# Kernel tuning notes

Hardware: AMD Instinct MI355X
Metric: run time of the kernel (lower is better)

## Reference

```python
import jax, jax.numpy as jnp
import numpy as np

N_WORD = 50000
N_DOC = 10000
E_WW = 800000
E_WD = 320000


def _sage(h_src, h_dst, src, dst, n_dst, W_self, W_neigh, b):
    # DGL SAGEConv('mean'): fc_self(h_dst) + fc_neigh(mean_{u in N(v)} h_u) + bias
    ones = jnp.ones((src.shape[0],), dtype=h_src.dtype)
    deg = jax.ops.segment_sum(ones, dst, num_segments=n_dst)            # [n_dst]
    agg = jax.ops.segment_sum(h_src[src], dst, num_segments=n_dst)      # [n_dst, d]
    mean = agg / jnp.maximum(deg, 1.0)[:, None]                          # zero for isolated
    return h_dst @ W_self + mean @ W_neigh + b


def _layer(xw, xd, edges, Ws, Wn, b):
    (ww_s, ww_d, wwr_s, wwr_d, wd_s, wd_d, wdr_s, wdr_d) = edges
    # relations targeting 'word': word2word, word2wordr, word2documentr
    h_ww = _sage(xw, xw, ww_s, ww_d, N_WORD, Ws[0], Wn[0], b[0])
    h_wwr = _sage(xw, xw, wwr_s, wwr_d, N_WORD, Ws[1], Wn[1], b[1])
    h_wdr = _sage(xd, xw, wdr_s, wdr_d, N_WORD, Ws[3], Wn[3], b[3])
    # relation targeting 'document': word2document
    h_wd = _sage(xw, xd, wd_s, wd_d, N_DOC, Ws[2], Wn[2], b[2])
    # HeteroGraphConv aggregate='stack' then torch.sum(dim=1) == sum over relations; then relu
    return jax.nn.relu(h_ww + h_wwr + h_wdr), jax.nn.relu(h_wd)


def setup_inputs() -> dict:
    key = jax.random.key(0)
    ks = jax.random.split(key, 20)
    d_in, d_h = 256, 128
    inp = {
        "x_word": jax.random.normal(ks[0], (N_WORD, d_in), jnp.float32),
        "x_doc": jax.random.normal(ks[1], (N_DOC, d_in), jnp.float32),
        "ww_src": jax.random.randint(ks[2], (E_WW,), 0, N_WORD, jnp.int32),
        "ww_dst": jax.random.randint(ks[3], (E_WW,), 0, N_WORD, jnp.int32),
        "wwr_src": jax.random.randint(ks[4], (E_WW,), 0, N_WORD, jnp.int32),
        "wwr_dst": jax.random.randint(ks[5], (E_WW,), 0, N_WORD, jnp.int32),
        "wd_src": jax.random.randint(ks[6], (E_WD,), 0, N_WORD, jnp.int32),
        "wd_dst": jax.random.randint(ks[7], (E_WD,), 0, N_DOC, jnp.int32),
        "wdr_src": jax.random.randint(ks[8], (E_WD,), 0, N_DOC, jnp.int32),
        "wdr_dst": jax.random.randint(ks[9], (E_WD,), 0, N_WORD, jnp.int32),
        "Wself1": jax.random.normal(ks[10], (4, d_in, d_h), jnp.float32) * (1.0 / np.sqrt(d_in)),
        "Wneigh1": jax.random.normal(ks[11], (4, d_in, d_h), jnp.float32) * (1.0 / np.sqrt(d_in)),
        "b1": jnp.zeros((4, d_h), jnp.float32),
        "Wself2": jax.random.normal(ks[12], (4, d_h, d_h), jnp.float32) * (1.0 / np.sqrt(d_h)),
        "Wneigh2": jax.random.normal(ks[13], (4, d_h, d_h), jnp.float32) * (1.0 / np.sqrt(d_h)),
        "b2": jnp.zeros((4, d_h), jnp.float32),
        "lin_w": jax.random.normal(ks[14], (1, d_h), jnp.float32) * (1.0 / np.sqrt(d_h)),
        "lin_b": jnp.ones((1,), jnp.float32),
    }
    return inp


def reference(x_word, x_doc, ww_src, ww_dst, wwr_src, wwr_dst, wd_src, wd_dst,
              wdr_src, wdr_dst, Wself1, Wneigh1, b1, Wself2, Wneigh2, b2, lin_w, lin_b):
    edges = (ww_src, ww_dst, wwr_src, wwr_dst, wd_src, wd_dst, wdr_src, wdr_dst)
    xw, xd = _layer(x_word, x_doc, edges, Wself1, Wneigh1, b1)
    xw, xd = _layer(xw, xd, edges, Wself2, Wneigh2, b2)
    out_w = jax.nn.sigmoid(xw @ lin_w.T + lin_b)  # [N_WORD, 1]
    out_d = jax.nn.sigmoid(xd @ lin_w.T + lin_b)  # [N_DOC, 1]
    return out_w, out_d
```

## Files before the change

kernel.cpp:

```cpp
#include <hip/hip_runtime.h>
#include <math.h>

#define N_WORD 50000
#define N_DOC  10000
#define E_WW   800000
#define E_WD   320000
#define D_IN   256
#define D_H    128

#define NPB    256
#define NBK_W  196
#define NBK_D  40
#define BKT    (3 * NBK_W + NBK_D)
#define EPB    8192
#define NBLK_WW 98
#define NBLK_WD 40
#define NBLK_TOT (2 * NBLK_WW + 2 * NBLK_WD)
#define PACK_BLKS 145

#define CAP_WW  4736
#define CAP_WDR 2176
#define CAP_WD  8960

#define WSTRIP ((N_WORD + 63) / 64)
#define DSTRIP ((N_DOC + 63) / 64)
#define NSTRIP (WSTRIP + DSTRIP)

typedef __attribute__((ext_vector_type(8))) short short8;
typedef __attribute__((ext_vector_type(4))) float f32x4;
typedef __attribute__((ext_vector_type(2))) float f32x2;

__device__ inline unsigned short f2bf(float f) {
  unsigned u = __float_as_uint(f);
  u = (u + 0x7fffu + ((u >> 16) & 1u)) >> 16;
  return (unsigned short)u;
}

__device__ inline float bflo(unsigned u) { return __uint_as_float(u << 16); }
__device__ inline float bfhi(unsigned u) { return __uint_as_float(u & 0xffff0000u); }

struct G6 { const short* B[6]; unsigned short* C[6]; };

#define BCH 16384
#define W2SZ 16384

template <int ABF, int K>
__device__ void gemm_body(const void* __restrict__ Aw, const void* __restrict__ Ad,
                          const G6& g, int blk, short* __restrict__ Bs) {
  constexpr int KT = K >> 5;
  constexpr int NCH = KT / 4;
  int tid = threadIdx.x;
  int wid = tid >> 6, lane = tid & 63;
  const void* A; int M, row0, h0, h1;
  if (blk < WSTRIP) { A = Aw; M = N_WORD; row0 = blk << 6; h0 = 0; h1 = 4; }
  else { A = Ad; M = N_DOC; row0 = (blk - WSTRIP) << 6; h0 = 4; h1 = 6; }
  int r = lane & 15, quad = lane >> 4;
  int m0 = row0 + wid * 16;
  int mA = m0 + r; if (mA >= M) mA = M - 1;
  short8 afr[KT];
  if (ABF) {
    const short* ap = (const short*)A + (size_t)mA * K + quad * 8;
#pragma unroll
    for (int kt = 0; kt < KT; ++kt) afr[kt] = *(const short8*)(ap + kt * 32);
  } else {
    const float* ap = (const float*)A + (size_t)mA * K + quad * 8;
#pragma unroll
    for (int kt = 0; kt < KT; ++kt) {
      float4 a0 = *(const float4*)(ap + kt * 32);
      float4 a1 = *(const float4*)(ap + kt * 32 + 4);
      short8 v;
      v[0] = (short)f2bf(a0.x); v[1] = (short)f2bf(a0.y);
      v[2] = (short)f2bf(a0.z); v[3] = (short)f2bf(a0.w);
      v[4] = (short)f2bf(a1.x); v[5] = (short)f2bf(a1.y);
      v[6] = (short)f2bf(a1.z); v[7] = (short)f2bf(a1.w);
      afr[kt] = v;
    }
  }
  for (int h = h0; h < h1; ++h) {
    const short* Bp = g.B[h];
    f32x4 acc[8];
#pragma unroll
    for (int nt = 0; nt < 8; ++nt) acc[nt] = (f32x4){0.f, 0.f, 0.f, 0.f};
    for (int c = 0; c < NCH; ++c) {
      const short* src = Bp + (size_t)c * BCH;
#pragma unroll
      for (int i = 0; i < 8; ++i) {
        int o = (i * 256 + tid) * 8;
        *(short8*)(Bs + o) = *(const short8*)(src + o);
      }
      __syncthreads();
#pragma unroll
      for (int ktl = 0; ktl < 4; ++ktl) {
        const short* bbase = Bs + ktl * 4096 + lane * 8;
#pragma unroll
        for (int nt = 0; nt < 8; ++nt) {
          short8 bf = *(const short8*)(bbase + nt * 512);
          acc[nt] = __builtin_amdgcn_mfma_f32_16x16x32_bf16(afr[c * 4 + ktl], bf, acc[nt], 0, 0, 0);
        }
      }
      __syncthreads();
    }
    unsigned short* C = g.C[h];
#pragma unroll
    for (int nt = 0; nt < 8; ++nt)
#pragma unroll
      for (int rr = 0; rr < 4; ++rr) {
        int row = m0 + quad * 4 + rr;
        if (row < M) C[(size_t)row * 128 + nt * 16 + r] = f2bf(acc[nt][rr]);
      }
  }
}

template <int NS>
__device__ void gemm2_fused(const unsigned* A0, const unsigned* A1,
                            const unsigned* A2, const unsigned* A3,
                            const short* B0, const short* B1,
                            const short* B2, const short* B3,
                            int M, int row0, const float* __restrict__ bias, int ob,
                            const float* __restrict__ lw, const float* __restrict__ lb,
                            float* __restrict__ out, short* __restrict__ Bs) {
  const unsigned* As[4] = {A0, A1, A2, A3};
  const short* Bm[4] = {B0, B1, B2, B3};
  int tid = threadIdx.x;
  int wid = tid >> 6, lane = tid & 63;
  int r = lane & 15, quad = lane >> 4;
  int m0 = row0 + wid * 16;
  int mA = m0 + r; if (mA >= M) mA = M - 1;
  short8 afr[NS][4];
#pragma unroll
  for (int s = 0; s < NS; ++s) {
    const short* ap = (const short*)As[s] + (size_t)mA * 128 + quad * 8;
#pragma unroll
    for (int kt = 0; kt < 4; ++kt) afr[s][kt] = *(const short8*)(ap + kt * 32);
  }
  f32x4 acc[8];
#pragma unroll
  for (int nt = 0; nt < 8; ++nt) acc[nt] = (f32x4){0.f, 0.f, 0.f, 0.f};
#pragma unroll
  for (int s = 0; s < NS; ++s) {
    const short* src = Bm[s];
#pragma unroll
    for (int i = 0; i < 8; ++i) {
      int o = (i * 256 + tid) * 8;
      *(short8*)(Bs + o) = *(const short8*)(src + o);
    }
    __syncthreads();
#pragma unroll
    for (int ktl = 0; ktl < 4; ++ktl) {
      const short* bbase = Bs + ktl * 4096 + lane * 8;
#pragma unroll
      for (int nt = 0; nt < 8; ++nt) {
        short8 bf = *(const short8*)(bbase + nt * 512);
        acc[nt] = __builtin_amdgcn_mfma_f32_16x16x32_bf16(afr[s][ktl], bf, acc[nt], 0, 0, 0);
      }
    }
    __syncthreads();
  }
  float bsv[8], lwv[8];
#pragma unroll
  for (int nt = 0; nt < 8; ++nt) { bsv[nt] = bias[nt * 16 + r]; lwv[nt] = lw[nt * 16 + r]; }
  float lbv = lb[0];
#pragma unroll
  for (int rr = 0; rr < 4; ++rr) {
    float p = 0.f;
#pragma unroll
    for (int nt = 0; nt < 8; ++nt) {
      float v = acc[nt][rr] + bsv[nt];
      v = fmaxf(v, 0.f);
      p += v * lwv[nt];
    }
    p += __shfl_xor(p, 1, 64);
    p += __shfl_xor(p, 2, 64);
    p += __shfl_xor(p, 4, 64);
    p += __shfl_xor(p, 8, 64);
    int row = m0 + quad * 4 + rr;
    if (r == 0 && row < M) out[ob + row] = 1.0f / (1.0f + expf(-(p + lbv)));
  }
}

__global__ __launch_bounds__(256, 2) void gemm2f_kernel(
    const unsigned* __restrict__ x1w, const unsigned* __restrict__ x1d,
    const unsigned* __restrict__ mww, const unsigned* __restrict__ mwwr,
    const unsigned* __restrict__ mwdr, const unsigned* __restrict__ mwd,
    const short* __restrict__ Bp2, const float* __restrict__ bsW,
    const float* __restrict__ bsD, const float* __restrict__ lw,
    const float* __restrict__ lb, float* __restrict__ out) {
  __shared__ short Bs[W2SZ];
  int blk = blockIdx.x;
  if (blk < WSTRIP)
    gemm2_fused<4>(x1w, mww, mwwr, mwdr,
                   Bp2, Bp2 + W2SZ, Bp2 + 2 * W2SZ, Bp2 + 4 * W2SZ,
                   N_WORD, blk << 6, bsW, 0, lw, lb, out, Bs);
  else
    gemm2_fused<2>(x1d, mwd, nullptr, nullptr,
                   Bp2 + 5 * W2SZ, Bp2 + 3 * W2SZ, nullptr, nullptr,
                   N_DOC, (blk - WSTRIP) << 6, bsD, N_WORD, lw, lb, out, Bs);
}

__global__ __launch_bounds__(256) void prep_kernel(
    const float* __restrict__ Ws1, const float* __restrict__ Wn1,
    const float* __restrict__ Ws2, const float* __restrict__ Wn2,
    short* __restrict__ Bp1, short* __restrict__ Bp2,
    const float* __restrict__ b1, const float* __restrict__ b2,
    float* __restrict__ bs1, float* __restrict__ bs2, int* __restrict__ bcnt,
    unsigned* __restrict__ zA, unsigned* __restrict__ zB,
    unsigned* __restrict__ zC, unsigned* __restrict__ zD,
    unsigned* __restrict__ zE, unsigned* __restrict__ zF) {
  int b = blockIdx.x;
  if (b == PACK_BLKS) {
    for (int i = threadIdx.x; i < BKT; i += 256) bcnt[i] = 0;
    if (threadIdx.x < 64) {
      zA[(size_t)N_WORD * 64 + threadIdx.x] = 0;
      zB[(size_t)N_WORD * 64 + threadIdx.x] = 0;
      zC[(size_t)N_WORD * 64 + threadIdx.x] = 0;
      zD[(size_t)N_DOC * 64 + threadIdx.x] = 0;
      zE[(size_t)N_WORD * 64 + threadIdx.x] = 0;
      zF[(size_t)N_DOC * 64 + threadIdx.x] = 0;
    }
    return;
  }
  int tid = b * 256 + threadIdx.x;
  const int L1T = 6 * 4096;
  const int L2T = 6 * 2048;
  if (tid >= L1T + L2T) {
    int t = tid - (L1T + L2T);
    if (t < 128) bs1[t] = b1[t] + b1[128 + t] + b1[384 + t];
    else if (t < 256) { int u = t - 128; bs2[u] = b2[u] + b2[128 + u] + b2[384 + u]; }
    return;
  }
  const float *src0, *src1 = nullptr, *src2 = nullptr;
  short* dstp;
  int kt, nt, lane;
  if (tid < L1T) {
    int mat = tid / 4096, rem = tid % 4096;
    kt = rem / 512; nt = (rem / 64) % 8; lane = rem % 64;
    const int W1 = 256 * 128;
    if (mat == 0) { src0 = Ws1; src1 = Ws1 + W1; src2 = Ws1 + 3 * W1; }
    else if (mat <= 4) src0 = Wn1 + (size_t)(mat - 1) * W1;
    else src0 = Ws1 + 2 * W1;
    dstp = Bp1 + (size_t)mat * W1 + ((size_t)(kt * 8 + nt) * 64 + lane) * 8;
  } else {
    int t2 = tid - L1T;
    int mat = t2 / 2048, rem = t2 % 2048;
    kt = rem / 512; nt = (rem / 64) % 8; lane = rem % 64;
    if (mat == 0) { src0 = Ws2; src1 = Ws2 + W2SZ; src2 = Ws2 + 3 * W2SZ; }
    else if (mat <= 4) src0 = Wn2 + (size_t)(mat - 1) * W2SZ;
    else src0 = Ws2 + 2 * W2SZ;
    dstp = Bp2 + (size_t)mat * W2SZ + ((size_t)(kt * 8 + nt) * 64 + lane) * 8;
  }
  int n = nt * 16 + (lane & 15);
  int kb = kt * 32 + (lane >> 4) * 8;
  short8 v;
#pragma unroll
  for (int j = 0; j < 8; ++j) {
    float f = src0[(size_t)(kb + j) * 128 + n];
    if (src1) f += src1[(size_t)(kb + j) * 128 + n] + src2[(size_t)(kb + j) * 128 + n];
    v[j] = (short)f2bf(f);
  }
  *(short8*)dstp = v;
}

__device__ inline void rel_map(int b, const int* wwd, const int* wwrd, const int* wdrd,
                               const int* wdd, const int*& dst, int& E, int& gbase, int& lb) {
  if (b < NBLK_WW) { dst = wwd; E = E_WW; gbase = 0; lb = b; }
  else if (b < 2 * NBLK_WW) { dst = wwrd; E = E_WW; gbase = NBK_W; lb = b - NBLK_WW; }
  else if (b < 2 * NBLK_WW + NBLK_WD) { dst = wdrd; E = E_WD; gbase = 2 * NBK_W; lb = b - 2 * NBLK_WW; }
  else { dst = wdd; E = E_WD; gbase = 3 * NBK_W; lb = b - 2 * NBLK_WW - NBLK_WD; }
}

struct BinLDS {
  unsigned buf[EPB];
  int hist[NBK_W];
  int lofs[NBK_W];
  int gofs[NBK_W];
  int lcur[NBK_W];
  int sm[256];
};

union FusedLDS {
  BinLDS bin;
  short bs[BCH];
};

__global__ __launch_bounds__(256, 4) void bin_gemm1(
    const int* wws, const int* wwd, const int* wwrs, const int* wwrd,
    const int* wdrs, const int* wdrd, const int* wds, const int* wdd,
    int* bcnt, unsigned* st_ww, unsigned* st_wwr, unsigned* st_wdr, unsigned* st_wd,
    const float* __restrict__ Aw, const float* __restrict__ Ad, G6 g) {
  __shared__ FusedLDS U;
  int b = blockIdx.x;
  if (b >= NBLK_TOT) {
    gemm_body<0, 256>(Aw, Ad, g, b - NBLK_TOT, U.bs);
    return;
  }
  BinLDS& L = U.bin;
  const int* dst; int E, gbase, lb;
  rel_map(b, wwd, wwrd, wdrd, wdd, dst, E, gbase, lb);
  const int* src; unsigned* st; int cap;
  if (b < NBLK_WW) { src = wws; st = st_ww; cap = CAP_WW; }
  else if (b < 2 * NBLK_WW) { src = wwrs; st = st_wwr; cap = CAP_WW; }
  else if (b < 2 * NBLK_WW + NBLK_WD) { src = wdrs; st = st_wdr; cap = CAP_WDR; }
  else { src = wds; st = st_wd; cap = CAP_WD; }
  int tid = threadIdx.x;
  int e0 = lb * EPB;
  int ecnt = E - e0; if (ecnt > EPB) ecnt = EPB;
  if (tid < NBK_W) L.hist[tid] = 0;
  __syncthreads();
  int dcache[EPB / 256];
#pragma unroll
  for (int k = 0; k < EPB / 256; ++k) {
    int i = e0 + k * 256 + tid;
    int d = (i < E) ? dst[i] : -1;
    dcache[k] = d;
    if (d >= 0) atomicAdd(&L.hist[d >> 8], 1);
  }
  __syncthreads();
  {
    int v = (tid < NBK_W) ? L.hist[tid] : 0;
    L.sm[tid] = v;
    __syncthreads();
    for (int o = 1; o < 256; o <<= 1) {
      int add = (tid >= o) ? L.sm[tid - o] : 0;
      __syncthreads();
      L.sm[tid] += add;
      __syncthreads();
    }
    if (tid < NBK_W) {
      int ex = L.sm[tid] - v;
      L.lofs[tid] = ex;
      L.lcur[tid] = ex;
      int base = v ? atomicAdd(&bcnt[gbase + tid], v) : 0;
      L.gofs[tid] = (int)((size_t)tid * cap) + base - ex;
    }
  }
  __syncthreads();
#pragma unroll
  for (int k = 0; k < EPB / 256; ++k) {
    int d = dcache[k];
    if (d >= 0) {
      int i = e0 + k * 256 + tid;
      int bk = d >> 8;
      int p = atomicAdd(&L.lcur[bk], 1);
      L.buf[p] = ((unsigned)bk << 24) | ((unsigned)(d & 255) << 16) |
                 (unsigned)(src[i] & 0xFFFF);
    }
  }
  __syncthreads();
#pragma unroll
  for (int k = 0; k < EPB / 256; ++k) {
    int p = k * 256 + tid;
    if (p < ecnt) {
      unsigned e = L.buf[p];
      st[L.gofs[e >> 24] + p] = e & 0x00FFFFFFu;
    }
  }
}

struct CSRB {
  const unsigned *st_ww, *st_wwr, *st_wdr, *st_wd;
  unsigned short *c_ww, *c_wwr, *c_wdr, *c_wd;
  int *rp_ww, *rp_wwr, *rp_wdr, *rp_wd;
  const int* bcnt;
};

__global__ __launch_bounds__(256) void place_kernel(CSRB q) {
  __shared__ int cnt[256], off[256], sm[256];
  int g = blockIdx.x;
  const unsigned* st; unsigned short* csr; int* rp; int relFirst, relLast, n, cap, Etot;
  if (g < NBK_W)            { st = q.st_ww;  csr = q.c_ww;  rp = q.rp_ww;  relFirst = 0;         relLast = NBK_W - 1;     n = N_WORD; cap = CAP_WW;  Etot = E_WW; }
  else if (g < 2 * NBK_W)   { st = q.st_wwr; csr = q.c_wwr; rp = q.rp_wwr; relFirst = NBK_W;     relLast = 2 * NBK_W - 1; n = N_WORD; cap = CAP_WW;  Etot = E_WW; }
  else if (g < 3 * NBK_W)   { st = q.st_wdr; csr = q.c_wdr; rp = q.rp_wdr; relFirst = 2 * NBK_W; relLast = 3 * NBK_W - 1; n = N_WORD; cap = CAP_WDR; Etot = E_WD; }
  else                      { st = q.st_wd;  csr = q.c_wd;  rp = q.rp_wd;  relFirst = 3 * NBK_W; relLast = BKT - 1;       n = N_DOC;  cap = CAP_WD;  Etot = E_WD; }
  int cb = g - relFirst;
  int tid = threadIdx.x;
  int v = (tid < cb) ? q.bcnt[relFirst + tid] : 0;
  sm[tid] = v;
  __syncthreads();
  for (int o = 128; o > 0; o >>= 1) {
    if (tid < o) sm[tid] += sm[tid + o];
    __syncthreads();
  }
  int bstart = sm[0];
  if (g == relLast && tid == 0) rp[n] = Etot;
  __syncthreads();
  int node_base = cb << 8;
  int node_cnt = n - node_base; if (node_cnt > NPB) node_cnt = NPB;
  int ecnt = q.bcnt[g];
  const unsigned* w = st + (size_t)cb * cap;
  cnt[tid] = 0;
  __syncthreads();
  for (int j = tid; j < ecnt; j += 256) atomicAdd(&cnt[w[j] >> 16], 1);
  __syncthreads();
  int c = cnt[tid];
  sm[tid] = c;
  __syncthreads();
  for (int o = 1; o < 256; o <<= 1) {
    int add = (tid >= o) ? sm[tid - o] : 0;
    __syncthreads();
    sm[tid] += add;
    __syncthreads();
  }
  int ex = sm[tid] - c;
  off[tid] = ex;
  if (tid < node_cnt) rp[node_base + tid] = bstart + ex;
  __syncthreads();
  for (int j = tid; j < ecnt; j += 256) {
    unsigned e = w[j];
    int p = atomicAdd(&off[e >> 16], 1);
    csr[bstart + p] = (unsigned short)(e & 0xFFFFu);
  }
}

__device__ inline void accum_rel4(const uint4* __restrict__ Y,
                                  const unsigned short* __restrict__ csr,
                                  int beg, int end, int lane, int r, int g,
                                  int zrow, f32x2* __restrict__ f) {
  int deg = end - beg;
  if (deg <= 0) return;
  f32x2 a0 = {0.f, 0.f}, a1 = a0, a2 = a0, a3 = a0;
  for (int base = beg; base < end; base += 64) {
    int cnt = end - base; if (cnt > 64) cnt = 64;
    int ld = base + lane;
    int idx = (ld < end) ? (int)csr[ld] : zrow;
    for (int j = 0; j < cnt; j += 16) {
      uint4 u[4];
#pragma unroll
      for (int t = 0; t < 4; ++t) {
        int sv = __shfl(idx, j + (t << 2) + g, 64);
        u[t] = Y[(unsigned)((sv << 4) + r)];
      }
#pragma unroll
      for (int t = 0; t < 4; ++t) {
        a0 += (f32x2){bflo(u[t].x), bfhi(u[t].x)};
        a1 += (f32x2){bflo(u[t].y), bfhi(u[t].y)};
        a2 += (f32x2){bflo(u[t].z), bfhi(u[t].z)};
        a3 += (f32x2){bflo(u[t].w), bfhi(u[t].w)};
      }
    }
  }
  float inv = 1.0f / (float)deg;
  f[0] += a0 * inv; f[1] += a1 * inv; f[2] += a2 * inv; f[3] += a3 * inv;
}

__global__ __launch_bounds__(256) void gather_all(
    const unsigned* __restrict__ y_ww, const unsigned* __restrict__ y_wwr,
    const unsigned* __restrict__ y_wdr, const unsigned* __restrict__ y_wd,
    const unsigned short* __restrict__ c_ww, const unsigned short* __restrict__ c_wwr,
    const unsigned short* __restrict__ c_wdr, const unsigned short* __restrict__ c_wd,
    const int* __restrict__ r_ww, const int* __restrict__ r_wwr,
    const int* __restrict__ r_wdr, const int* __restrict__ r_wd,
    const unsigned* __restrict__ tW, const unsigned* __restrict__ tD,
    const float* __restrict__ bW, const float* __restrict__ bD,
    unsigned* __restrict__ oW16, unsigned* __restrict__ oD16) {
  int gn = (blockIdx.x << 2) + (threadIdx.x >> 6);
  if (gn >= N_WORD + N_DOC) return;
  int lane = threadIdx.x & 63;
  int r = lane & 15, g = lane >> 4;
  f32x2 f[4];
#pragma unroll
  for (int i = 0; i < 4; ++i) f[i] = (f32x2){0.f, 0.f};
  bool isw = (gn < N_WORD);
  int node = isw ? gn : gn - N_WORD;
  if (isw) {
    accum_rel4((const uint4*)y_ww, c_ww, r_ww[node], r_ww[node + 1], lane, r, g, N_WORD, f);
    accum_rel4((const uint4*)y_wwr, c_wwr, r_wwr[node], r_wwr[node + 1], lane, r, g, N_WORD, f);
    accum_rel4((const uint4*)y_wdr, c_wdr, r_wdr[node], r_wdr[node + 1], lane, r, g, N_DOC, f);
  } else {
    accum_rel4((const uint4*)y_wd, c_wd, r_wd[node], r_wd[node + 1], lane, r, g, N_WORD, f);
  }
#pragma unroll
  for (int i = 0; i < 4; ++i) {
    f[i].x += __shfl_xor(f[i].x, 16, 64);
    f[i].y += __shfl_xor(f[i].y, 16, 64);
    f[i].x += __shfl_xor(f[i].x, 32, 64);
    f[i].y += __shfl_xor(f[i].y, 32, 64);
  }
  const unsigned* tS = isw ? tW : tD;
  uint4 tu = ((const uint4*)tS)[(unsigned)((node << 4) + r)];
  const float* bs = isw ? bW : bD;
  float4 bv0 = ((const float4*)bs)[2 * r];
  float4 bv1 = ((const float4*)bs)[2 * r + 1];
  f[0].x = fmaxf(f[0].x + bflo(tu.x) + bv0.x, 0.f);
  f[0].y = fmaxf(f[0].y + bfhi(tu.x) + bv0.y, 0.f);
  f[1].x = fmaxf(f[1].x + bflo(tu.y) + bv0.z, 0.f);
  f[1].y = fmaxf(f[1].y + bfhi(tu.y) + bv0.w, 0.f);
  f[2].x = fmaxf(f[2].x + bflo(tu.z) + bv1.x, 0.f);
  f[2].y = fmaxf(f[2].y + bfhi(tu.z) + bv1.y, 0.f);
  f[3].x = fmaxf(f[3].x + bflo(tu.w) + bv1.z, 0.f);
  f[3].y = fmaxf(f[3].y + bfhi(tu.w) + bv1.w, 0.f);
  if (g == 0) {
    uint4 pk;
    pk.x = (unsigned)f2bf(f[0].x) | ((unsigned)f2bf(f[0].y) << 16);
    pk.y = (unsigned)f2bf(f[1].x) | ((unsigned)f2bf(f[1].y) << 16);
    pk.z = (unsigned)f2bf(f[2].x) | ((unsigned)f2bf(f[2].y) << 16);
    pk.w = (unsigned)f2bf(f[3].x) | ((unsigned)f2bf(f[3].y) << 16);
    unsigned* o = isw ? oW16 : oD16;
    ((uint4*)o)[(unsigned)((node << 4) + r)] = pk;
  }
}

__device__ inline void mean_write(int node, int lane, int r, int g,
                                  f32x2* __restrict__ A, unsigned* __restrict__ mT) {
#pragma unroll
  for (int i = 0; i < 4; ++i) {
    A[i].x += __shfl_xor(A[i].x, 16, 64);
    A[i].y += __shfl_xor(A[i].y, 16, 64);
    A[i].x += __shfl_xor(A[i].x, 32, 64);
    A[i].y += __shfl_xor(A[i].y, 32, 64);
  }
  if (g == 0) {
    uint4 pk;
    pk.x = (unsigned)f2bf(A[0].x) | ((unsigned)f2bf(A[0].y) << 16);
    pk.y = (unsigned)f2bf(A[1].x) | ((unsigned)f2bf(A[1].y) << 16);
    pk.z = (unsigned)f2bf(A[2].x) | ((unsigned)f2bf(A[2].y) << 16);
    pk.w = (unsigned)f2bf(A[3].x) | ((unsigned)f2bf(A[3].y) << 16);
    ((uint4*)mT)[(unsigned)((node << 4) + r)] = pk;
  }
}

__global__ __launch_bounds__(256) void gather_mean(
    const unsigned* __restrict__ yW, const unsigned* __restrict__ yD,
    const unsigned short* __restrict__ c_ww, const unsigned short* __restrict__ c_wwr,
    const unsigned short* __restrict__ c_wdr, const unsigned short* __restrict__ c_wd,
    const int* __restrict__ r_ww, const int* __restrict__ r_wwr,
    const int* __restrict__ r_wdr, const int* __restrict__ r_wd,
    unsigned* __restrict__ mWW, unsigned* __restrict__ mWWR,
    unsigned* __restrict__ mWDR, unsigned* __restrict__ mWD) {
  int gn = (blockIdx.x << 2) + (threadIdx.x >> 6);
  if (gn >= N_WORD + N_DOC) return;
  int lane = threadIdx.x & 63;
  int r = lane & 15, g = lane >> 4;
  bool isw = (gn < N_WORD);
  int node = isw ? gn : gn - N_WORD;
  f32x2 A[4];
  if (isw) {
#pragma unroll
    for (int i = 0; i < 4; ++i) A[i] = (f32x2){0.f, 0.f};
    accum_rel4((const uint4*)yW, c_ww, r_ww[node], r_ww[node + 1], lane, r, g, N_WORD, A);
    mean_write(node, lane, r, g, A, mWW);
#pragma unroll
    for (int i = 0; i < 4; ++i) A[i] = (f32x2){0.f, 0.f};
    accum_rel4((const uint4*)yW, c_wwr, r_wwr[node], r_wwr[node + 1], lane, r, g, N_WORD, A);
    mean_write(node, lane, r, g, A, mWWR);
#pragma unroll
    for (int i = 0; i < 4; ++i) A[i] = (f32x2){0.f, 0.f};
    accum_rel4((const uint4*)yD, c_wdr, r_wdr[node], r_wdr[node + 1], lane, r, g, N_DOC, A);
    mean_write(node, lane, r, g, A, mWDR);
  } else {
#pragma unroll
    for (int i = 0; i < 4; ++i) A[i] = (f32x2){0.f, 0.f};
    accum_rel4((const uint4*)yW, c_wd, r_wd[node], r_wd[node + 1], lane, r, g, N_WORD, A);
    mean_write(node, lane, r, g, A, mWD);
  }
}

extern "C" void kernel_launch(void* const* d_in, const int* in_sizes, int n_in,
                              void* d_out, int out_size, void* d_ws, size_t ws_size,
                              hipStream_t stream) {
  const float* xw      = (const float*)d_in[0];
  const float* xd      = (const float*)d_in[1];
  const int*   ww_src  = (const int*)d_in[2];
  const int*   ww_dst  = (const int*)d_in[3];
  const int*   wwr_src = (const int*)d_in[4];
  const int*   wwr_dst = (const int*)d_in[5];
  const int*   wd_src  = (const int*)d_in[6];
  const int*   wd_dst  = (const int*)d_in[7];
  const int*   wdr_src = (const int*)d_in[8];
  const int*   wdr_dst = (const int*)d_in[9];
  const float* Ws1     = (const float*)d_in[10];
  const float* Wn1     = (const float*)d_in[11];
  const float* b1      = (const float*)d_in[12];
  const float* Ws2     = (const float*)d_in[13];
  const float* Wn2     = (const float*)d_in[14];
  const float* b2      = (const float*)d_in[15];
  const float* lin_w   = (const float*)d_in[16];
  const float* lin_b   = (const float*)d_in[17];
  float* out = (float*)d_out;

  char* p = (char*)d_ws;
  auto alloc = [&](size_t nbytes) {
    char* r = p;
    p += (nbytes + 255) & ~(size_t)255;
    return r;
  };
  unsigned* twA  = (unsigned*)alloc((size_t)N_WORD * D_H * 2);
  unsigned* tdA  = (unsigned*)alloc((size_t)N_DOC * D_H * 2);
  unsigned* xw1B = (unsigned*)alloc((size_t)N_WORD * D_H * 2 + 256);
  unsigned* xd1B = (unsigned*)alloc((size_t)N_DOC * D_H * 2 + 256);
  unsigned* yB0 = (unsigned*)alloc((size_t)N_WORD * D_H * 2 + 256);
  unsigned* yB1 = (unsigned*)alloc(((size_t)NBK_W * CAP_WDR + (size_t)NBK_D * CAP_WD) * 4);
  unsigned* yB2 = (unsigned*)alloc((size_t)N_WORD * D_H * 2 + 256);
  unsigned* ydB = (unsigned*)alloc((size_t)N_DOC * D_H * 2 + 256);
  unsigned short* csr_ww  = (unsigned short*)alloc((size_t)E_WW * 2);
  unsigned short* csr_wwr = (unsigned short*)alloc((size_t)E_WW * 2);
  unsigned short* csr_wdr = (unsigned short*)alloc((size_t)E_WD * 2);
  unsigned short* csr_wd  = (unsigned short*)alloc((size_t)E_WD * 2);
  int* rp_ww  = (int*)alloc((size_t)(N_WORD + 1) * 4);
  int* rp_wwr = (int*)alloc((size_t)(N_WORD + 1) * 4);
  int* rp_wdr = (int*)alloc((size_t)(N_WORD + 1) * 4);
  int* rp_wd  = (int*)alloc((size_t)(N_DOC + 1) * 4);
  short* Bp1 = (short*)alloc((size_t)6 * 256 * 128 * 2);
  short* Bp2 = (short*)alloc((size_t)6 * 128 * 128 * 2);
  int* bcnt  = (int*)alloc((size_t)BKT * 4);
  float* bs1 = (float*)alloc(D_H * 4);
  float* bs2 = (float*)alloc(D_H * 4);
  unsigned* yBX = (unsigned*)alloc((size_t)N_WORD * D_H * 2 + 256);
  unsigned* st_ww  = yB0;
  unsigned* st_wwr = st_ww + (size_t)NBK_W * CAP_WW;
  unsigned* st_wdr = yB1;
  unsigned* st_wd  = st_wdr + (size_t)NBK_W * CAP_WDR;

  const int W1 = 256 * 128;

  prep_kernel<<<PACK_BLKS + 1, 256, 0, stream>>>(
      Ws1, Wn1, Ws2, Wn2, Bp1, Bp2, b1, b2, bs1, bs2, bcnt,
      yB2, xw1B, yBX, ydB, yB0, xd1B);

  G6 g1;
  g1.B[0] = Bp1 + 0 * W1; g1.C[0] = (unsigned short*)twA;
  g1.B[1] = Bp1 + 1 * W1; g1.C[1] = (unsigned short*)yB2;
  g1.B[2] = Bp1 + 2 * W1; g1.C[2] = (unsigned short*)xw1B;
  g1.B[3] = Bp1 + 3 * W1; g1.C[3] = (unsigned short*)yBX;
  g1.B[4] = Bp1 + 5 * W1; g1.C[4] = (unsigned short*)tdA;
  g1.B[5] = Bp1 + 4 * W1; g1.C[5] = (unsigned short*)ydB;
  bin_gemm1<<<NBLK_TOT + NSTRIP, 256, 0, stream>>>(
      ww_src, ww_dst, wwr_src, wwr_dst, wdr_src, wdr_dst, wd_src, wd_dst,
      bcnt, st_ww, st_wwr, st_wdr, st_wd, xw, xd, g1);

  CSRB q;
  q.st_ww = st_ww; q.st_wwr = st_wwr; q.st_wdr = st_wdr; q.st_wd = st_wd;
  q.c_ww = csr_ww; q.c_wwr = csr_wwr; q.c_wdr = csr_wdr; q.c_wd = csr_wd;
  q.rp_ww = rp_ww; q.rp_wwr = rp_wwr; q.rp_wdr = rp_wdr; q.rp_wd = rp_wd;
  q.bcnt = bcnt;
  place_kernel<<<BKT, 256, 0, stream>>>(q);

  gather_all<<<(N_WORD + N_DOC + 3) / 4, 256, 0, stream>>>(
      yB2, xw1B, ydB, yBX, csr_ww, csr_wwr, csr_wdr, csr_wd,
      rp_ww, rp_wwr, rp_wdr, rp_wd, twA, tdA, bs1, b1 + 256,
      yB0, xd1B);

  gather_mean<<<(N_WORD + N_DOC + 3) / 4, 256, 0, stream>>>(
      yB0, xd1B, csr_ww, csr_wwr, csr_wdr, csr_wd,
      rp_ww, rp_wwr, rp_wdr, rp_wd,
      yB2 , xw1B , yBX , ydB );

  gemm2f_kernel<<<NSTRIP, 256, 0, stream>>>(
      yB0, xd1B, yB2, xw1B, yBX, ydB, Bp2, bs2, b2 + 256,
      lin_w, lin_b, out);
}
```

Before: 359.7 us.

## Split layer-1 word gather across relations and add bf16 combine kernel

The fused layer-1 gather, where each word wave walked three relations in sequence, is replaced by a kernel that gives the ww+wdr relations and the wwr relation to separate blocks. Each writes a bf16 partial sum, and a new elementwise combine kernel adds the two partials, the self term and the bias, then applies relu. The aim is more parallelism and shorter per-wave latency chains in the gather. The cost is an extra launch, an extra 12.8MB round trip of bf16 partials, and extra bf16 rounding of the partial sums.

```diff
diff --git a/kernel.cpp b/kernel.cpp
--- a/kernel.cpp
+++ b/kernel.cpp
@@ -25,6 +25,9 @@
 #define WSTRIP ((N_WORD + 63) / 64)
 #define DSTRIP ((N_DOC + 63) / 64)
 #define NSTRIP (WSTRIP + DSTRIP)
+
+#define WBP (N_WORD / 4)
+#define DBP (N_DOC / 4)
 
 typedef __attribute__((ext_vector_type(8))) short short8;
 typedef __attribute__((ext_vector_type(4))) float f32x4;
@@ -442,64 +445,7 @@
   f[0] += a0 * inv; f[1] += a1 * inv; f[2] += a2 * inv; f[3] += a3 * inv;
 }
 
-__global__ __launch_bounds__(256) void gather_all(
-    const unsigned* __restrict__ y_ww, const unsigned* __restrict__ y_wwr,
-    const unsigned* __restrict__ y_wdr, const unsigned* __restrict__ y_wd,
-    const unsigned short* __restrict__ c_ww, const unsigned short* __restrict__ c_wwr,
-    const unsigned short* __restrict__ c_wdr, const unsigned short* __restrict__ c_wd,
-    const int* __restrict__ r_ww, const int* __restrict__ r_wwr,
-    const int* __restrict__ r_wdr, const int* __restrict__ r_wd,
-    const unsigned* __restrict__ tW, const unsigned* __restrict__ tD,
-    const float* __restrict__ bW, const float* __restrict__ bD,
-    unsigned* __restrict__ oW16, unsigned* __restrict__ oD16) {
-  int gn = (blockIdx.x << 2) + (threadIdx.x >> 6);
-  if (gn >= N_WORD + N_DOC) return;
-  int lane = threadIdx.x & 63;
-  int r = lane & 15, g = lane >> 4;
-  f32x2 f[4];
-#pragma unroll
-  for (int i = 0; i < 4; ++i) f[i] = (f32x2){0.f, 0.f};
-  bool isw = (gn < N_WORD);
-  int node = isw ? gn : gn - N_WORD;
-  if (isw) {
-    accum_rel4((const uint4*)y_ww, c_ww, r_ww[node], r_ww[node + 1], lane, r, g, N_WORD, f);
-    accum_rel4((const uint4*)y_wwr, c_wwr, r_wwr[node], r_wwr[node + 1], lane, r, g, N_WORD, f);
-    accum_rel4((const uint4*)y_wdr, c_wdr, r_wdr[node], r_wdr[node + 1], lane, r, g, N_DOC, f);
-  } else {
-    accum_rel4((const uint4*)y_wd, c_wd, r_wd[node], r_wd[node + 1], lane, r, g, N_WORD, f);
-  }
-#pragma unroll
-  for (int i = 0; i < 4; ++i) {
-    f[i].x += __shfl_xor(f[i].x, 16, 64);
-    f[i].y += __shfl_xor(f[i].y, 16, 64);
-    f[i].x += __shfl_xor(f[i].x, 32, 64);
-    f[i].y += __shfl_xor(f[i].y, 32, 64);
-  }
-  const unsigned* tS = isw ? tW : tD;
-  uint4 tu = ((const uint4*)tS)[(unsigned)((node << 4) + r)];
-  const float* bs = isw ? bW : bD;
-  float4 bv0 = ((const float4*)bs)[2 * r];
-  float4 bv1 = ((const float4*)bs)[2 * r + 1];
-  f[0].x = fmaxf(f[0].x + bflo(tu.x) + bv0.x, 0.f);
-  f[0].y = fmaxf(f[0].y + bfhi(tu.x) + bv0.y, 0.f);
-  f[1].x = fmaxf(f[1].x + bflo(tu.y) + bv0.z, 0.f);
-  f[1].y = fmaxf(f[1].y + bfhi(tu.y) + bv0.w, 0.f);
-  f[2].x = fmaxf(f[2].x + bflo(tu.z) + bv1.x, 0.f);
-  f[2].y = fmaxf(f[2].y + bfhi(tu.z) + bv1.y, 0.f);
-  f[3].x = fmaxf(f[3].x + bflo(tu.w) + bv1.z, 0.f);
-  f[3].y = fmaxf(f[3].y + bfhi(tu.w) + bv1.w, 0.f);
-  if (g == 0) {
-    uint4 pk;
-    pk.x = (unsigned)f2bf(f[0].x) | ((unsigned)f2bf(f[0].y) << 16);
-    pk.y = (unsigned)f2bf(f[1].x) | ((unsigned)f2bf(f[1].y) << 16);
-    pk.z = (unsigned)f2bf(f[2].x) | ((unsigned)f2bf(f[2].y) << 16);
-    pk.w = (unsigned)f2bf(f[3].x) | ((unsigned)f2bf(f[3].y) << 16);
-    unsigned* o = isw ? oW16 : oD16;
-    ((uint4*)o)[(unsigned)((node << 4) + r)] = pk;
-  }
-}
-
-__device__ inline void mean_write(int node, int lane, int r, int g,
+__device__ inline void mean_write(int node, int r, int g,
                                   f32x2* __restrict__ A, unsigned* __restrict__ mT) {
 #pragma unroll
   for (int i = 0; i < 4; ++i) {
@@ -516,6 +462,90 @@
     pk.w = (unsigned)f2bf(A[3].x) | ((unsigned)f2bf(A[3].y) << 16);
     ((uint4*)mT)[(unsigned)((node << 4) + r)] = pk;
   }
+}
+
+__global__ __launch_bounds__(256) void gather_rel1(
+    const unsigned* __restrict__ y_ww, const unsigned* __restrict__ y_wwr,
+    const unsigned* __restrict__ y_wdr, const unsigned* __restrict__ y_wd,
+    const unsigned short* __restrict__ c_ww, const unsigned short* __restrict__ c_wwr,
+    const unsigned short* __restrict__ c_wdr, const unsigned short* __restrict__ c_wd,
+    const int* __restrict__ r_ww, const int* __restrict__ r_wwr,
+    const int* __restrict__ r_wdr, const int* __restrict__ r_wd,
+    const unsigned* __restrict__ tD, const float* __restrict__ bD,
+    unsigned* __restrict__ P1, unsigned* __restrict__ P2,
+    unsigned* __restrict__ oD16) {
+  int b = blockIdx.x;
+  int lane = threadIdx.x & 63;
+  int r = lane & 15, g = lane >> 4;
+  f32x2 f[4];
+#pragma unroll
+  for (int i = 0; i < 4; ++i) f[i] = (f32x2){0.f, 0.f};
+  if (b < WBP) {
+    int node = (b << 2) + (threadIdx.x >> 6);
+    accum_rel4((const uint4*)y_ww, c_ww, r_ww[node], r_ww[node + 1], lane, r, g, N_WORD, f);
+    accum_rel4((const uint4*)y_wdr, c_wdr, r_wdr[node], r_wdr[node + 1], lane, r, g, N_DOC, f);
+    mean_write(node, r, g, f, P1);
+  } else if (b < 2 * WBP) {
+    int node = ((b - WBP) << 2) + (threadIdx.x >> 6);
+    accum_rel4((const uint4*)y_wwr, c_wwr, r_wwr[node], r_wwr[node + 1], lane, r, g, N_WORD, f);
+    mean_write(node, r, g, f, P2);
+  } else {
+    int node = ((b - 2 * WBP) << 2) + (threadIdx.x >> 6);
+    accum_rel4((const uint4*)y_wd, c_wd, r_wd[node], r_wd[node + 1], lane, r, g, N_WORD, f);
+#pragma unroll
+    for (int i = 0; i < 4; ++i) {
+      f[i].x += __shfl_xor(f[i].x, 16, 64);
+      f[i].y += __shfl_xor(f[i].y, 16, 64);
+      f[i].x += __shfl_xor(f[i].x, 32, 64);
+      f[i].y += __shfl_xor(f[i].y, 32, 64);
+    }
+    uint4 tu = ((const uint4*)tD)[(unsigned)((node << 4) + r)];
+    float4 bv0 = ((const float4*)bD)[2 * r];
+    float4 bv1 = ((const float4*)bD)[2 * r + 1];
+    f[0].x = fmaxf(f[0].x + bflo(tu.x) + bv0.x, 0.f);
+    f[0].y = fmaxf(f[0].y + bfhi(tu.x) + bv0.y, 0.f);
+    f[1].x = fmaxf(f[1].x + bflo(tu.y) + bv0.z, 0.f);
+    f[1].y = fmaxf(f[1].y + bfhi(tu.y) + bv0.w, 0.f);
+    f[2].x = fmaxf(f[2].x + bflo(tu.z) + bv1.x, 0.f);
+    f[2].y = fmaxf(f[2].y + bfhi(tu.z) + bv1.y, 0.f);
+    f[3].x = fmaxf(f[3].x + bflo(tu.w) + bv1.z, 0.f);
+    f[3].y = fmaxf(f[3].y + bfhi(tu.w) + bv1.w, 0.f);
+    if (g == 0) {
+      uint4 pk;
+      pk.x = (unsigned)f2bf(f[0].x) | ((unsigned)f2bf(f[0].y) << 16);
+      pk.y = (unsigned)f2bf(f[1].x) | ((unsigned)f2bf(f[1].y) << 16);
+      pk.z = (unsigned)f2bf(f[2].x) | ((unsigned)f2bf(f[2].y) << 16);
+      pk.w = (unsigned)f2bf(f[3].x) | ((unsigned)f2bf(f[3].y) << 16);
+      ((uint4*)oD16)[(unsigned)((node << 4) + r)] = pk;
+    }
+  }
+}
+
+__global__ __launch_bounds__(256) void combine1(
+    const unsigned* tW, const unsigned* P1, const unsigned* P2,
+    const float* __restrict__ bsW, unsigned* oW16) {
+  int idx = blockIdx.x * 256 + threadIdx.x;
+  if (idx >= N_WORD * 16) return;
+  int r = idx & 15;
+  uint4 p1 = ((const uint4*)P1)[idx];
+  uint4 p2 = ((const uint4*)P2)[idx];
+  uint4 tu = ((const uint4*)tW)[idx];
+  float4 bv0 = ((const float4*)bsW)[2 * r];
+  float4 bv1 = ((const float4*)bsW)[2 * r + 1];
+  float v0 = fmaxf(bflo(p1.x) + bflo(p2.x) + bflo(tu.x) + bv0.x, 0.f);
+  float v1 = fmaxf(bfhi(p1.x) + bfhi(p2.x) + bfhi(tu.x) + bv0.y, 0.f);
+  float v2 = fmaxf(bflo(p1.y) + bflo(p2.y) + bflo(tu.y) + bv0.z, 0.f);
+  float v3 = fmaxf(bfhi(p1.y) + bfhi(p2.y) + bfhi(tu.y) + bv0.w, 0.f);
+  float v4 = fmaxf(bflo(p1.z) + bflo(p2.z) + bflo(tu.z) + bv1.x, 0.f);
+  float v5 = fmaxf(bfhi(p1.z) + bfhi(p2.z) + bfhi(tu.z) + bv1.y, 0.f);
+  float v6 = fmaxf(bflo(p1.w) + bflo(p2.w) + bflo(tu.w) + bv1.z, 0.f);
+  float v7 = fmaxf(bfhi(p1.w) + bfhi(p2.w) + bfhi(tu.w) + bv1.w, 0.f);
+  uint4 pk;
+  pk.x = (unsigned)f2bf(v0) | ((unsigned)f2bf(v1) << 16);
+  pk.y = (unsigned)f2bf(v2) | ((unsigned)f2bf(v3) << 16);
+  pk.z = (unsigned)f2bf(v4) | ((unsigned)f2bf(v5) << 16);
+  pk.w = (unsigned)f2bf(v6) | ((unsigned)f2bf(v7) << 16);
+  ((uint4*)oW16)[idx] = pk;
 }
 
 __global__ __launch_bounds__(256) void gather_mean(
@@ -537,20 +567,20 @@
 #pragma unroll
     for (int i = 0; i < 4; ++i) A[i] = (f32x2){0.f, 0.f};
     accum_rel4((const uint4*)yW, c_ww, r_ww[node], r_ww[node + 1], lane, r, g, N_WORD, A);
-    mean_write(node, lane, r, g, A, mWW);
+    mean_write(node, r, g, A, mWW);
 #pragma unroll
     for (int i = 0; i < 4; ++i) A[i] = (f32x2){0.f, 0.f};
     accum_rel4((const uint4*)yW, c_wwr, r_wwr[node], r_wwr[node + 1], lane, r, g, N_WORD, A);
-    mean_write(node, lane, r, g, A, mWWR);
+    mean_write(node, r, g, A, mWWR);
 #pragma unroll
     for (int i = 0; i < 4; ++i) A[i] = (f32x2){0.f, 0.f};
     accum_rel4((const uint4*)yD, c_wdr, r_wdr[node], r_wdr[node + 1], lane, r, g, N_DOC, A);
-    mean_write(node, lane, r, g, A, mWDR);
+    mean_write(node, r, g, A, mWDR);
   } else {
 #pragma unroll
     for (int i = 0; i < 4; ++i) A[i] = (f32x2){0.f, 0.f};
     accum_rel4((const uint4*)yW, c_wd, r_wd[node], r_wd[node + 1], lane, r, g, N_WORD, A);
-    mean_write(node, lane, r, g, A, mWD);
+    mean_write(node, r, g, A, mWD);
   }
 }
 
@@ -605,6 +635,7 @@
   float* bs1 = (float*)alloc(D_H * 4);
   float* bs2 = (float*)alloc(D_H * 4);
   unsigned* yBX = (unsigned*)alloc((size_t)N_WORD * D_H * 2 + 256);
+  unsigned* P2  = (unsigned*)alloc((size_t)N_WORD * D_H * 2);
   unsigned* st_ww  = yB0;
   unsigned* st_wwr = st_ww + (size_t)NBK_W * CAP_WW;
   unsigned* st_wdr = yB1;
@@ -634,10 +665,13 @@
   q.bcnt = bcnt;
   place_kernel<<<BKT, 256, 0, stream>>>(q);
 
-  gather_all<<<(N_WORD + N_DOC + 3) / 4, 256, 0, stream>>>(
+  gather_rel1<<<2 * WBP + DBP, 256, 0, stream>>>(
       yB2, xw1B, ydB, yBX, csr_ww, csr_wwr, csr_wdr, csr_wd,
-      rp_ww, rp_wwr, rp_wdr, rp_wd, twA, tdA, bs1, b1 + 256,
-      yB0, xd1B);
+      rp_ww, rp_wwr, rp_wdr, rp_wd, tdA, b1 + 256,
+      yB0 , P2, xd1B);
+
+  combine1<<<(N_WORD * 16 + 255) / 256, 256, 0, stream>>>(
+      twA, yB0, P2, bs1, yB0);
 
   gather_mean<<<(N_WORD + N_DOC + 3) / 4, 256, 0, stream>>>(
       yB0, xd1B, csr_ww, csr_wwr, csr_wdr, csr_wd,
```

New measurement: 363.9 us. No clear change (+1.2%).

## Split layer-1 features into column halves for cache-friendly second-layer gather

Applied to the files above, without the earlier changes.

Layer-1 outputs are stored as two separate bf16 half-width arrays (columns 0-63 and 64-127) instead of one 128-column array. The mean-gather kernel now launches twice as many blocks, with each block gathering one half using 8-lane row segments. This halves the working set each block's random gathers touch, so more of it can stay in cache. The second-layer GEMM reads its A fragments from the split buffers. The cost is extra shuffle reductions, repeated CSR index reads for both halves, and reworked buffer aliasing.

```diff
diff --git a/kernel.cpp b/kernel.cpp
--- a/kernel.cpp
+++ b/kernel.cpp
@@ -25,6 +25,8 @@
 #define WSTRIP ((N_WORD + 63) / 64)
 #define DSTRIP ((N_DOC + 63) / 64)
 #define NSTRIP (WSTRIP + DSTRIP)
+
+#define GMB    ((N_WORD + N_DOC + 3) / 4)
 
 typedef __attribute__((ext_vector_type(8))) short short8;
 typedef __attribute__((ext_vector_type(4))) float f32x4;
@@ -111,15 +113,15 @@
   }
 }
 
+struct A2 { const unsigned *L[4], *H[4]; };
+
 template <int NS>
-__device__ void gemm2_fused(const unsigned* A0, const unsigned* A1,
-                            const unsigned* A2, const unsigned* A3,
+__device__ void gemm2_fused(const A2& a,
                             const short* B0, const short* B1,
                             const short* B2, const short* B3,
                             int M, int row0, const float* __restrict__ bias, int ob,
                             const float* __restrict__ lw, const float* __restrict__ lb,
                             float* __restrict__ out, short* __restrict__ Bs) {
-  const unsigned* As[4] = {A0, A1, A2, A3};
   const short* Bm[4] = {B0, B1, B2, B3};
   int tid = threadIdx.x;
   int wid = tid >> 6, lane = tid & 63;
@@ -129,9 +131,12 @@
   short8 afr[NS][4];
 #pragma unroll
   for (int s = 0; s < NS; ++s) {
-    const short* ap = (const short*)As[s] + (size_t)mA * 128 + quad * 8;
-#pragma unroll
-    for (int kt = 0; kt < 4; ++kt) afr[s][kt] = *(const short8*)(ap + kt * 32);
+    const short* apL = (const short*)a.L[s] + (size_t)mA * 64 + quad * 8;
+    const short* apH = (const short*)a.H[s] + (size_t)mA * 64 + quad * 8;
+    afr[s][0] = *(const short8*)apL;
+    afr[s][1] = *(const short8*)(apL + 32);
+    afr[s][2] = *(const short8*)apH;
+    afr[s][3] = *(const short8*)(apH + 32);
   }
   f32x4 acc[8];
 #pragma unroll
@@ -179,21 +184,16 @@
 }
 
 __global__ __launch_bounds__(256, 2) void gemm2f_kernel(
-    const unsigned* __restrict__ x1w, const unsigned* __restrict__ x1d,
-    const unsigned* __restrict__ mww, const unsigned* __restrict__ mwwr,
-    const unsigned* __restrict__ mwdr, const unsigned* __restrict__ mwd,
-    const short* __restrict__ Bp2, const float* __restrict__ bsW,
+    A2 aw, A2 ad, const short* __restrict__ Bp2, const float* __restrict__ bsW,
     const float* __restrict__ bsD, const float* __restrict__ lw,
     const float* __restrict__ lb, float* __restrict__ out) {
   __shared__ short Bs[W2SZ];
   int blk = blockIdx.x;
   if (blk < WSTRIP)
-    gemm2_fused<4>(x1w, mww, mwwr, mwdr,
-                   Bp2, Bp2 + W2SZ, Bp2 + 2 * W2SZ, Bp2 + 4 * W2SZ,
+    gemm2_fused<4>(aw, Bp2, Bp2 + W2SZ, Bp2 + 2 * W2SZ, Bp2 + 4 * W2SZ,
                    N_WORD, blk << 6, bsW, 0, lw, lb, out, Bs);
   else
-    gemm2_fused<2>(x1d, mwd, nullptr, nullptr,
-                   Bp2 + 5 * W2SZ, Bp2 + 3 * W2SZ, nullptr, nullptr,
+    gemm2_fused<2>(ad, Bp2 + 5 * W2SZ, Bp2 + 3 * W2SZ, nullptr, nullptr,
                    N_DOC, (blk - WSTRIP) << 6, bsD, N_WORD, lw, lb, out, Bs);
 }
 
@@ -205,7 +205,8 @@
     float* __restrict__ bs1, float* __restrict__ bs2, int* __restrict__ bcnt,
     unsigned* __restrict__ zA, unsigned* __restrict__ zB,
     unsigned* __restrict__ zC, unsigned* __restrict__ zD,
-    unsigned* __restrict__ zE, unsigned* __restrict__ zF) {
+    unsigned* __restrict__ hA, unsigned* __restrict__ hB,
+    unsigned* __restrict__ hC, unsigned* __restrict__ hD) {
   int b = blockIdx.x;
   if (b == PACK_BLKS) {
     for (int i = threadIdx.x; i < BKT; i += 256) bcnt[i] = 0;
@@ -214,8 +215,12 @@
       zB[(size_t)N_WORD * 64 + threadIdx.x] = 0;
       zC[(size_t)N_WORD * 64 + threadIdx.x] = 0;
       zD[(size_t)N_DOC * 64 + threadIdx.x] = 0;
-      zE[(size_t)N_WORD * 64 + threadIdx.x] = 0;
-      zF[(size_t)N_DOC * 64 + threadIdx.x] = 0;
+    }
+    if (threadIdx.x < 32) {
+      hA[(size_t)N_WORD * 32 + threadIdx.x] = 0;
+      hB[(size_t)N_WORD * 32 + threadIdx.x] = 0;
+      hC[(size_t)N_DOC * 32 + threadIdx.x] = 0;
+      hD[(size_t)N_DOC * 32 + threadIdx.x] = 0;
     }
     return;
   }
@@ -442,6 +447,55 @@
   f[0] += a0 * inv; f[1] += a1 * inv; f[2] += a2 * inv; f[3] += a3 * inv;
 }
 
+__device__ inline void accum_rel4h(const uint4* __restrict__ Y,
+                                   const unsigned short* __restrict__ csr,
+                                   int beg, int end, int lane, int r2, int g2,
+                                   int zrow, f32x2* __restrict__ f) {
+  int deg = end - beg;
+  if (deg <= 0) return;
+  f32x2 a0 = {0.f, 0.f}, a1 = a0, a2 = a0, a3 = a0;
+  for (int base = beg; base < end; base += 64) {
+    int cnt = end - base; if (cnt > 64) cnt = 64;
+    int ld = base + lane;
+    int idx = (ld < end) ? (int)csr[ld] : zrow;
+    for (int j = 0; j < cnt; j += 32) {
+      uint4 u[4];
+#pragma unroll
+      for (int t = 0; t < 4; ++t) {
+        int sv = __shfl(idx, j + (t << 3) + g2, 64);
+        u[t] = Y[(unsigned)((sv << 3) + r2)];
+      }
+#pragma unroll
+      for (int t = 0; t < 4; ++t) {
+        a0 += (f32x2){bflo(u[t].x), bfhi(u[t].x)};
+        a1 += (f32x2){bflo(u[t].y), bfhi(u[t].y)};
+        a2 += (f32x2){bflo(u[t].z), bfhi(u[t].z)};
+        a3 += (f32x2){bflo(u[t].w), bfhi(u[t].w)};
+      }
+    }
+  }
+  float inv = 1.0f / (float)deg;
+  f[0] += a0 * inv; f[1] += a1 * inv; f[2] += a2 * inv; f[3] += a3 * inv;
+}
+
+__device__ inline void mean_write_h(int node, int r2, int g2,
+                                    f32x2* __restrict__ A, unsigned* __restrict__ mT) {
+#pragma unroll
+  for (int i = 0; i < 4; ++i) {
+    A[i].x += __shfl_xor(A[i].x, 8, 64);  A[i].y += __shfl_xor(A[i].y, 8, 64);
+    A[i].x += __shfl_xor(A[i].x, 16, 64); A[i].y += __shfl_xor(A[i].y, 16, 64);
+    A[i].x += __shfl_xor(A[i].x, 32, 64); A[i].y += __shfl_xor(A[i].y, 32, 64);
+  }
+  if (g2 == 0) {
+    uint4 pk;
+    pk.x = (unsigned)f2bf(A[0].x) | ((unsigned)f2bf(A[0].y) << 16);
+    pk.y = (unsigned)f2bf(A[1].x) | ((unsigned)f2bf(A[1].y) << 16);
+    pk.z = (unsigned)f2bf(A[2].x) | ((unsigned)f2bf(A[2].y) << 16);
+    pk.w = (unsigned)f2bf(A[3].x) | ((unsigned)f2bf(A[3].y) << 16);
+    ((uint4*)mT)[(unsigned)((node << 3) + r2)] = pk;
+  }
+}
+
 __global__ __launch_bounds__(256) void gather_all(
     const unsigned* __restrict__ y_ww, const unsigned* __restrict__ y_wwr,
     const unsigned* __restrict__ y_wdr, const unsigned* __restrict__ y_wd,
@@ -451,7 +505,8 @@
     const int* __restrict__ r_wdr, const int* __restrict__ r_wd,
     const unsigned* __restrict__ tW, const unsigned* __restrict__ tD,
     const float* __restrict__ bW, const float* __restrict__ bD,
-    unsigned* __restrict__ oW16, unsigned* __restrict__ oD16) {
+    unsigned* __restrict__ oWLo, unsigned* __restrict__ oWHi,
+    unsigned* __restrict__ oDLo, unsigned* __restrict__ oDHi) {
   int gn = (blockIdx.x << 2) + (threadIdx.x >> 6);
   if (gn >= N_WORD + N_DOC) return;
   int lane = threadIdx.x & 63;
@@ -494,63 +549,49 @@
     pk.y = (unsigned)f2bf(f[1].x) | ((unsigned)f2bf(f[1].y) << 16);
     pk.z = (unsigned)f2bf(f[2].x) | ((unsigned)f2bf(f[2].y) << 16);
     pk.w = (unsigned)f2bf(f[3].x) | ((unsigned)f2bf(f[3].y) << 16);
-    unsigned* o = isw ? oW16 : oD16;
-    ((uint4*)o)[(unsigned)((node << 4) + r)] = pk;
-  }
-}
-
-__device__ inline void mean_write(int node, int lane, int r, int g,
-                                  f32x2* __restrict__ A, unsigned* __restrict__ mT) {
-#pragma unroll
-  for (int i = 0; i < 4; ++i) {
-    A[i].x += __shfl_xor(A[i].x, 16, 64);
-    A[i].y += __shfl_xor(A[i].y, 16, 64);
-    A[i].x += __shfl_xor(A[i].x, 32, 64);
-    A[i].y += __shfl_xor(A[i].y, 32, 64);
-  }
-  if (g == 0) {
-    uint4 pk;
-    pk.x = (unsigned)f2bf(A[0].x) | ((unsigned)f2bf(A[0].y) << 16);
-    pk.y = (unsigned)f2bf(A[1].x) | ((unsigned)f2bf(A[1].y) << 16);
-    pk.z = (unsigned)f2bf(A[2].x) | ((unsigned)f2bf(A[2].y) << 16);
-    pk.w = (unsigned)f2bf(A[3].x) | ((unsigned)f2bf(A[3].y) << 16);
-    ((uint4*)mT)[(unsigned)((node << 4) + r)] = pk;
-  }
-}
+    unsigned* o;
+    if (isw) o = (r < 8) ? oWLo : oWHi;
+    else     o = (r < 8) ? oDLo : oDHi;
+    ((uint4*)o)[(unsigned)((node << 3) + (r & 7))] = pk;
+  }
+}
+
+struct MT { const unsigned *yW, *yD; unsigned *mWW, *mWWR, *mWDR, *mWD; };
 
 __global__ __launch_bounds__(256) void gather_mean(
-    const unsigned* __restrict__ yW, const unsigned* __restrict__ yD,
+    MT lo, MT hi,
     const unsigned short* __restrict__ c_ww, const unsigned short* __restrict__ c_wwr,
     const unsigned short* __restrict__ c_wdr, const unsigned short* __restrict__ c_wd,
     const int* __restrict__ r_ww, const int* __restrict__ r_wwr,
-    const int* __restrict__ r_wdr, const int* __restrict__ r_wd,
-    unsigned* __restrict__ mWW, unsigned* __restrict__ mWWR,
-    unsigned* __restrict__ mWDR, unsigned* __restrict__ mWD) {
-  int gn = (blockIdx.x << 2) + (threadIdx.x >> 6);
+    const int* __restrict__ r_wdr, const int* __restrict__ r_wd) {
+  int b = blockIdx.x;
+  bool isLo = (b < GMB);
+  const MT& m = isLo ? lo : hi;
+  int gn = ((isLo ? b : b - GMB) << 2) + (threadIdx.x >> 6);
   if (gn >= N_WORD + N_DOC) return;
   int lane = threadIdx.x & 63;
-  int r = lane & 15, g = lane >> 4;
+  int r2 = lane & 7, g2 = lane >> 3;
   bool isw = (gn < N_WORD);
   int node = isw ? gn : gn - N_WORD;
   f32x2 A[4];
   if (isw) {
 #pragma unroll
     for (int i = 0; i < 4; ++i) A[i] = (f32x2){0.f, 0.f};
-    accum_rel4((const uint4*)yW, c_ww, r_ww[node], r_ww[node + 1], lane, r, g, N_WORD, A);
-    mean_write(node, lane, r, g, A, mWW);
+    accum_rel4h((const uint4*)m.yW, c_ww, r_ww[node], r_ww[node + 1], lane, r2, g2, N_WORD, A);
+    mean_write_h(node, r2, g2, A, m.mWW);
 #pragma unroll
     for (int i = 0; i < 4; ++i) A[i] = (f32x2){0.f, 0.f};
-    accum_rel4((const uint4*)yW, c_wwr, r_wwr[node], r_wwr[node + 1], lane, r, g, N_WORD, A);
-    mean_write(node, lane, r, g, A, mWWR);
+    accum_rel4h((const uint4*)m.yW, c_wwr, r_wwr[node], r_wwr[node + 1], lane, r2, g2, N_WORD, A);
+    mean_write_h(node, r2, g2, A, m.mWWR);
 #pragma unroll
     for (int i = 0; i < 4; ++i) A[i] = (f32x2){0.f, 0.f};
-    accum_rel4((const uint4*)yD, c_wdr, r_wdr[node], r_wdr[node + 1], lane, r, g, N_DOC, A);
-    mean_write(node, lane, r, g, A, mWDR);
+    accum_rel4h((const uint4*)m.yD, c_wdr, r_wdr[node], r_wdr[node + 1], lane, r2, g2, N_DOC, A);
+    mean_write_h(node, r2, g2, A, m.mWDR);
   } else {
 #pragma unroll
     for (int i = 0; i < 4; ++i) A[i] = (f32x2){0.f, 0.f};
-    accum_rel4((const uint4*)yW, c_wd, r_wd[node], r_wd[node + 1], lane, r, g, N_WORD, A);
-    mean_write(node, lane, r, g, A, mWD);
+    accum_rel4h((const uint4*)m.yW, c_wd, r_wd[node], r_wd[node + 1], lane, r2, g2, N_WORD, A);
+    mean_write_h(node, r2, g2, A, m.mWD);
   }
 }
 
@@ -586,11 +627,14 @@
   unsigned* twA  = (unsigned*)alloc((size_t)N_WORD * D_H * 2);
   unsigned* tdA  = (unsigned*)alloc((size_t)N_DOC * D_H * 2);
   unsigned* xw1B = (unsigned*)alloc((size_t)N_WORD * D_H * 2 + 256);
-  unsigned* xd1B = (unsigned*)alloc((size_t)N_DOC * D_H * 2 + 256);
-  unsigned* yB0 = (unsigned*)alloc((size_t)N_WORD * D_H * 2 + 256);
+  unsigned* yB2  = (unsigned*)alloc((size_t)N_WORD * D_H * 2 + 256);
+  unsigned* yBX  = (unsigned*)alloc((size_t)N_WORD * D_H * 2 + 256);
+  unsigned* ydB  = (unsigned*)alloc((size_t)N_DOC * D_H * 2 + 256);
+  unsigned* yB0L  = (unsigned*)alloc((size_t)N_WORD * 64 * 2 + 128);
+  unsigned* yB0H  = (unsigned*)alloc((size_t)N_WORD * 64 * 2 + 128);
+  unsigned* xd1BL = (unsigned*)alloc((size_t)N_DOC * 64 * 2 + 128);
+  unsigned* xd1BH = (unsigned*)alloc((size_t)N_DOC * 64 * 2 + 128);
   unsigned* yB1 = (unsigned*)alloc(((size_t)NBK_W * CAP_WDR + (size_t)NBK_D * CAP_WD) * 4);
-  unsigned* yB2 = (unsigned*)alloc((size_t)N_WORD * D_H * 2 + 256);
-  unsigned* ydB = (unsigned*)alloc((size_t)N_DOC * D_H * 2 + 256);
   unsigned short* csr_ww  = (unsigned short*)alloc((size_t)E_WW * 2);
   unsigned short* csr_wwr = (unsigned short*)alloc((size_t)E_WW * 2);
   unsigned short* csr_wdr = (unsigned short*)alloc((size_t)E_WD * 2);
@@ -604,17 +648,20 @@
   int* bcnt  = (int*)alloc((size_t)BKT * 4);
   float* bs1 = (float*)alloc(D_H * 4);
   float* bs2 = (float*)alloc(D_H * 4);
-  unsigned* yBX = (unsigned*)alloc((size_t)N_WORD * D_H * 2 + 256);
-  unsigned* st_ww  = yB0;
-  unsigned* st_wwr = st_ww + (size_t)NBK_W * CAP_WW;
+  unsigned* st_ww  = yB0L;
+  unsigned* st_wwr = yB0H;
   unsigned* st_wdr = yB1;
   unsigned* st_wd  = st_wdr + (size_t)NBK_W * CAP_WDR;
+  unsigned* mWWL  = yB2;  unsigned* mWWH  = yB2 + (size_t)N_WORD * 32;
+  unsigned* mWWRL = xw1B; unsigned* mWWRH = xw1B + (size_t)N_WORD * 32;
+  unsigned* mWDRL = yBX;  unsigned* mWDRH = yBX + (size_t)N_WORD * 32;
+  unsigned* mWDL  = ydB;  unsigned* mWDH  = ydB + (size_t)N_DOC * 32;
 
   const int W1 = 256 * 128;
 
   prep_kernel<<<PACK_BLKS + 1, 256, 0, stream>>>(
       Ws1, Wn1, Ws2, Wn2, Bp1, Bp2, b1, b2, bs1, bs2, bcnt,
-      yB2, xw1B, yBX, ydB, yB0, xd1B);
+      yB2, xw1B, yBX, ydB, yB0L, yB0H, xd1BL, xd1BH);
 
   G6 g1;
   g1.B[0] = Bp1 + 0 * W1; g1.C[0] = (unsigned short*)twA;
@@ -634,17 +681,25 @@
   q.bcnt = bcnt;
   place_kernel<<<BKT, 256, 0, stream>>>(q);
 
-  gather_all<<<(N_WORD + N_DOC + 3) / 4, 256, 0, stream>>>(
+  gather_all<<<GMB, 256, 0, stream>>>(
       yB2, xw1B, ydB, yBX, csr_ww, csr_wwr, csr_wdr, csr_wd,
       rp_ww, rp_wwr, rp_wdr, rp_wd, twA, tdA, bs1, b1 + 256,
-      yB0, xd1B);
-
-  gather_mean<<<(N_WORD + N_DOC + 3) / 4, 256, 0, stream>>>(
-      yB0, xd1B, csr_ww, csr_wwr, csr_wdr, csr_wd,
-      rp_ww, rp_wwr, rp_wdr, rp_wd,
-      yB2 , xw1B , yBX , ydB );
-
+      yB0L, yB0H, xd1BL, xd1BH);
+
+  MT lo, hi;
+  lo.yW = yB0L; lo.yD = xd1BL;
+  lo.mWW = mWWL; lo.mWWR = mWWRL; lo.mWDR = mWDRL; lo.mWD = mWDL;
+  hi.yW = yB0H; hi.yD = xd1BH;
+  hi.mWW = mWWH; hi.mWWR = mWWRH; hi.mWDR = mWDRH; hi.mWD = mWDH;
+  gather_mean<<<2 * GMB, 256, 0, stream>>>(
+      lo, hi, csr_ww, csr_wwr, csr_wdr, csr_wd,
+      rp_ww, rp_wwr, rp_wdr, rp_wd);
+
+  A2 aw, ad;
+  aw.L[0] = yB0L;  aw.L[1] = mWWL;  aw.L[2] = mWWRL; aw.L[3] = mWDRL;
+  aw.H[0] = yB0H;  aw.H[1] = mWWH;  aw.H[2] = mWWRH; aw.H[3] = mWDRH;
+  ad.L[0] = xd1BL; ad.L[1] = mWDL;  ad.L[2] = nullptr; ad.L[3] = nullptr;
+  ad.H[0] = xd1BH; ad.H[1] = mWDH;  ad.H[2] = nullptr; ad.H[3] = nullptr;
   gemm2f_kernel<<<NSTRIP, 256, 0, stream>>>(
-      yB0, xd1B, yB2, xw1B, yBX, ydB, Bp2, bs2, b2 + 256,
-      lin_w, lin_b, out);
-}
+      aw, ad, Bp2, bs2, b2 + 256, lin_w, lin_b, out);
+}
```

Measured after the change: 394.0 us. +9.5%, slower.
